# Kernel tuning notes

Hardware: AMD Instinct MI355X
Metric: run time of the kernel (lower is better)

The kernel has to match this reference:

```python
import jax, jax.numpy as jnp
import numpy as np

INPUTS = 128        # raw inputs
HIDDEN = 256
OUTPUTS = 32
NETWORKS = 64
K = 32              # max_incoming_connections
INPUTS_T = INPUTS + 2                 # + zero-bias and one-bias neurons
NODES = HIDDEN + OUTPUTS              # sequentially computed neurons
NEURONS = INPUTS_T + HIDDEN + OUTPUTS
BATCH = 1024


def setup_inputs() -> dict:
    key = jax.random.key(0)
    k1, k2, k3 = jax.random.split(key, 3)
    x = jax.random.normal(k1, (BATCH, INPUTS), dtype=jnp.float32)
    W = jax.random.normal(k2, (INPUTS_T + HIDDEN, NODES), dtype=jnp.float32)
    networks_weights = jax.random.uniform(k3, (NETWORKS,), dtype=jnp.float32)
    # connections[n, i, k] < min(INPUTS_T + i - 1, INPUTS_T + HIDDEN), as in init_connections
    rng = np.random.default_rng(0)
    upper = np.minimum(INPUTS_T + np.arange(NODES) - 1, INPUTS_T + HIDDEN)
    raw = rng.integers(0, 1 << 30, size=(NETWORKS, NODES, K))
    connections = jnp.asarray((raw % upper[None, :, None]).astype(np.int32))
    return {"x": x, "W": W, "networks_weights": networks_weights,
            "connections": connections}


def _forward(x, W, networks_weights, connections):
    B = x.shape[0]
    # append zero-bias and one-bias input neurons
    inp = jnp.concatenate(
        [x, jnp.zeros((B, 1), x.dtype), jnp.ones((B, 1), x.dtype)], axis=1)
    post = jnp.concatenate([inp, jnp.zeros((B, NODES), x.dtype)], axis=1)  # [B, neurons]
    post = jnp.tile(post[:, None, :], (1, NETWORKS, 1))  # [B, networks, neurons]

    conns_per_node = jnp.transpose(connections, (1, 0, 2))  # [nodes, networks, K]
    node_ids = jnp.arange(NODES)

    def step(post, xs):
        idx, node = xs                                   # idx: [networks, K]
        gidx = jnp.broadcast_to(idx[None], (B, NETWORKS, K))
        vals = jnp.take_along_axis(post, gidx, axis=2)   # [B, networks, K]
        w = W[idx, node]                                  # [networks, K]
        out = jnp.sum(w[None] * vals, axis=2)             # [B, networks]
        act = jax.nn.leaky_relu(out)                      # slope 0.01, matches torch
        post = post.at[:, :, INPUTS_T + node].set(act)
        return post, None

    post, _ = jax.lax.scan(step, post, (conns_per_node, node_ids))
    outs = post[:, :, -OUTPUTS:]                          # [B, networks, outputs]
    wsoft = jax.nn.softmax(networks_weights)              # [networks]
    return jnp.einsum('n,bno->bo', wsoft, outs)


def reference(x, W, networks_weights, connections):
    return _forward(x, W, networks_weights, connections)
```

## Files before the change

### kernel.cpp

```cpp
#include <hip/hip_runtime.h>
#include <math.h>

#define NETS   64
#define NNODES 288
#define NHID   256
#define NOUT   32
#define KCON   32
#define NBATCH 1024
#define TILE   32

#ifdef __has_builtin
#if __has_builtin(__builtin_amdgcn_permlane32_swap)
#define HAVE_PLSWAP 1
#endif
#endif

__device__ __forceinline__ float xor32_sum(float a) {
#ifdef HAVE_PLSWAP
    auto r = __builtin_amdgcn_permlane32_swap(__float_as_uint(a), __float_as_uint(a),
                                              false, false);
    return __uint_as_float(r[0]) + __uint_as_float(r[1]);
#else
    return a + __shfl_xor(a, 32, 64);
#endif
}

__global__ __launch_bounds__(256) void prep_wg(const float* __restrict__ W,
                                               const int* __restrict__ conn,
                                               float* __restrict__ Wg) {
    int g = blockIdx.x * 256 + threadIdx.x;
    int node = (g >> 5) % NNODES;
    Wg[g] = W[(size_t)conn[g] * NNODES + node];
}

__global__ __launch_bounds__(256) void prep_xt(const float* __restrict__ x,
                                               float* __restrict__ xT) {
    int g = blockIdx.x * 256 + threadIdx.x;
    int b = g >> 7, r = g & 127;
    xT[(size_t)r * NBATCH + b] = x[g];
}

__global__ __launch_bounds__(64) void unn_main(const float* __restrict__ xT,
                                               const int* __restrict__ conn,
                                               const float* __restrict__ Wg,
                                               float* __restrict__ outs) {
    __shared__ float st[(130 + NHID) * TILE];
    const int lane = threadIdx.x;
    const int p    = lane & 15;
    const int s    = (lane >> 4) & 1;
    const int kh   = lane >> 5;
    const int net  = blockIdx.x >> 5;
    const int b0   = (blockIdx.x & 31) * TILE;

    for (int i = lane; i < 128 * TILE / 4; i += 64) {
        int row = i >> 3, c4 = i & 7;
        float4 v = *(const float4*)(xT + (size_t)row * NBATCH + b0 + c4 * 4);
        *(float4*)(st + row * TILE + c4 * 4) = v;
    }
    if (lane < TILE) {
        st[128 * TILE + lane] = 0.0f;
        st[129 * TILE + lane] = 1.0f;
    }
    __syncthreads();

    const size_t nb = (size_t)net * NNODES * KCON + s * KCON + kh * 16;
    const int*   cp  = conn + nb;
    const float* wp  = Wg   + nb;
    const float* stp = st + 2 * p;

    int4   ic0, ic1, ic2, ic3, in0, in1, in2, in3;
    float4 wc0, wc1, wc2, wc3, wn0, wn1, wn2, wn3;

#define PREF(I0,I1,I2,I3,W0,W1,W2,W3, nd) {                               \
    const int4*   ip = (const int4*)(cp + (size_t)(nd) * KCON);           \
    const float4* fp = (const float4*)(wp + (size_t)(nd) * KCON);         \
    I0 = ip[0]; I1 = ip[1]; I2 = ip[2]; I3 = ip[3];                       \
    W0 = fp[0]; W1 = fp[1]; W2 = fp[2]; W3 = fp[3]; }

#define G1(ii, ww) { float2 v = *(const float2*)(stp + ((ii) << 5));      \
    ax = fmaf((ww), v.x, ax); ay = fmaf((ww), v.y, ay); }

#define GATH(IV, WV) G1((IV).x, (WV).x) G1((IV).y, (WV).y)                \
                     G1((IV).z, (WV).z) G1((IV).w, (WV).w)

#define BODY(I0,I1,I2,I3,W0,W1,W2,W3, nd) {                               \
    float ax = 0.f, ay = 0.f;                                             \
    GATH(I0, W0) GATH(I1, W1) GATH(I2, W2) GATH(I3, W3)                   \
    ax = xor32_sum(ax);                                                   \
    ay = xor32_sum(ay);                                                   \
    float vx = fmaxf(ax, 0.01f * ax);                                     \
    float vy = fmaxf(ay, 0.01f * ay);                                     \
    if (kh == 0) {                                                        \
        int node = (nd) + s;                                              \
        if ((nd) < NHID)                                                  \
            *(float2*)(st + (130 + node) * TILE + 2 * p) = make_float2(vx, vy); \
        else                                                              \
            *(float2*)(outs + ((size_t)net * NOUT + (node - NHID)) * NBATCH    \
                       + b0 + 2 * p) = make_float2(vx, vy);               \
    } }

    PREF(ic0,ic1,ic2,ic3,wc0,wc1,wc2,wc3, 0)
    for (int nd = 0; nd < NNODES; nd += 4) {
        PREF(in0,in1,in2,in3,wn0,wn1,wn2,wn3, nd + 2)
        BODY(ic0,ic1,ic2,ic3,wc0,wc1,wc2,wc3, nd)
        int nd2 = (nd + 4 < NNODES) ? nd + 4 : NNODES - 2;
        PREF(ic0,ic1,ic2,ic3,wc0,wc1,wc2,wc3, nd2)
        BODY(in0,in1,in2,in3,wn0,wn1,wn2,wn3, nd + 2)
    }
#undef PREF
#undef G1
#undef GATH
#undef BODY
}

__global__ __launch_bounds__(64) void unn_reduce(const float* __restrict__ nw,
                                                 const float* __restrict__ outs,
                                                 float* __restrict__ out) {
    __shared__ float sw[NETS];
    int t  = threadIdx.x;
    int o  = blockIdx.x & 31;
    int bt = blockIdx.x >> 5;
    float v = nw[t];
    float m = v;
    #pragma unroll
    for (int off = 32; off; off >>= 1) m = fmaxf(m, __shfl_xor(m, off, 64));
    float e = __expf(v - m);
    float ssum = e;
    #pragma unroll
    for (int off = 32; off; off >>= 1) ssum += __shfl_xor(ssum, off, 64);
    sw[t] = e / ssum;
    __syncthreads();

    int bb = bt * 64 + t;
    float acc = 0.f;
    #pragma unroll 8
    for (int n = 0; n < NETS; ++n)
        acc = fmaf(sw[n], outs[((size_t)n * NOUT + o) * NBATCH + bb], acc);
    out[(size_t)bb * NOUT + o] = acc;
}

extern "C" void kernel_launch(void* const* d_in, const int* in_sizes, int n_in,
                              void* d_out, int out_size, void* d_ws, size_t ws_size,
                              hipStream_t stream) {
    const float* x    = (const float*)d_in[0];
    const float* W    = (const float*)d_in[1];
    const float* nw   = (const float*)d_in[2];
    const int*   conn = (const int*)d_in[3];
    float* out = (float*)d_out;

    char* ws = (char*)d_ws;
    float* Wg   = (float*)(ws);
    float* xT   = (float*)(ws + 2359296);
    float* outs = (float*)(ws + 2359296 + 524288);

    prep_wg <<<dim3((NETS*NNODES*KCON)/256), dim3(256), 0, stream>>>(W, conn, Wg);
    prep_xt <<<dim3((NBATCH*128)/256),       dim3(256), 0, stream>>>(x, xT);
    unn_main<<<dim3(NETS * (NBATCH/TILE)),   dim3(64),  0, stream>>>(xT, conn, Wg, outs);
    unn_reduce<<<dim3(512),                  dim3(64),  0, stream>>>(nw, outs, out);
}
```

Before: 164.4 us.

## Restructure sequential network kernel with packed metadata, smaller batch tile, deeper prefetch

Packs connection offsets and gathered weights into one interleaved int2 metadata array, so each lane loads byte offsets and weights together instead of from two streams. Halves the batch tile to 16, which doubles the block count, and splits the K reduction four ways with permlane16 and permlane32 swaps. Adds a three-deep prefetch of that metadata and an XCD-aware block remap. Folds the bias rows into the transpose kernel and adds a bf16 output fallback for when the workspace is too small, which costs precision on that path.

```diff
diff --git a/kernel.cpp b/kernel.cpp
--- a/kernel.cpp
+++ b/kernel.cpp
@@ -1,5 +1,4 @@
 #include <hip/hip_runtime.h>
-#include <math.h>
 
 #define NETS   64
 #define NNODES 288
@@ -7,16 +6,31 @@
 #define NOUT   32
 #define KCON   32
 #define NBATCH 1024
-#define TILE   32
-
-#ifdef __has_builtin
+#define TILE   16
+#define NPAIR  144
+#define ROWB   (TILE * 4)
+#define LDSZ   (386 * ROWB)
+
+#if defined(__has_builtin)
+#if __has_builtin(__builtin_amdgcn_permlane16_swap)
+#define HAVE_PL16 1
+#endif
 #if __has_builtin(__builtin_amdgcn_permlane32_swap)
-#define HAVE_PLSWAP 1
-#endif
-#endif
-
-__device__ __forceinline__ float xor32_sum(float a) {
-#ifdef HAVE_PLSWAP
+#define HAVE_PL32 1
+#endif
+#endif
+
+__device__ __forceinline__ float xor16_add(float a) {
+#ifdef HAVE_PL16
+    auto r = __builtin_amdgcn_permlane16_swap(__float_as_uint(a), __float_as_uint(a),
+                                              false, false);
+    return __uint_as_float(r[0]) + __uint_as_float(r[1]);
+#else
+    return a + __shfl_xor(a, 16, 64);
+#endif
+}
+__device__ __forceinline__ float xor32_add(float a) {
+#ifdef HAVE_PL32
     auto r = __builtin_amdgcn_permlane32_swap(__float_as_uint(a), __float_as_uint(a),
                                               false, false);
     return __uint_as_float(r[0]) + __uint_as_float(r[1]);
@@ -25,102 +39,121 @@
 #endif
 }
 
-__global__ __launch_bounds__(256) void prep_wg(const float* __restrict__ W,
-                                               const int* __restrict__ conn,
-                                               float* __restrict__ Wg) {
+__device__ __forceinline__ unsigned f2bf(float f) {
+    unsigned b = __float_as_uint(f);
+    return (b + 0x7FFFu + ((b >> 16) & 1u)) >> 16;
+}
+__device__ __forceinline__ float bf2f(unsigned short u) {
+    return __uint_as_float(((unsigned)u) << 16);
+}
+
+__global__ __launch_bounds__(256) void prep_meta(const float* __restrict__ W,
+                                                 const int* __restrict__ conn,
+                                                 int2* __restrict__ meta) {
     int g = blockIdx.x * 256 + threadIdx.x;
-    int node = (g >> 5) % NNODES;
-    Wg[g] = W[(size_t)conn[g] * NNODES + node];
+    int net = g / 9216;
+    int rem = g - net * 9216;
+    int node = rem >> 5, k = rem & 31;
+    int idx = conn[g];
+    float w = W[(size_t)idx * NNODES + node];
+    int didx = net * 9216 + (node >> 1) * 64 + (node & 1) * 32 + (k >> 3) * 8 + (k & 7);
+    meta[didx] = make_int2(idx * ROWB, __float_as_int(w));
 }
 
 __global__ __launch_bounds__(256) void prep_xt(const float* __restrict__ x,
                                                float* __restrict__ xT) {
     int g = blockIdx.x * 256 + threadIdx.x;
-    int b = g >> 7, r = g & 127;
-    xT[(size_t)r * NBATCH + b] = x[g];
-}
-
+    int r = g >> 10, b = g & 1023;
+    float v = (r < 128) ? x[(size_t)b * 128 + r] : ((r == 128) ? 0.0f : 1.0f);
+    xT[(size_t)r * NBATCH + b] = v;
+}
+
+template <bool F32OUT>
 __global__ __launch_bounds__(64) void unn_main(const float* __restrict__ xT,
-                                               const int* __restrict__ conn,
-                                               const float* __restrict__ Wg,
-                                               float* __restrict__ outs) {
-    __shared__ float st[(130 + NHID) * TILE];
+                                               const int2* __restrict__ meta,
+                                               void* __restrict__ outsv) {
+    __shared__ float Hf[LDSZ / 4];
+    char* Hl = (char*)Hf;
     const int lane = threadIdx.x;
-    const int p    = lane & 15;
-    const int s    = (lane >> 4) & 1;
-    const int kh   = lane >> 5;
-    const int net  = blockIdx.x >> 5;
-    const int b0   = (blockIdx.x & 31) * TILE;
-
-    for (int i = lane; i < 128 * TILE / 4; i += 64) {
-        int row = i >> 3, c4 = i & 7;
-        float4 v = *(const float4*)(xT + (size_t)row * NBATCH + b0 + c4 * 4);
-        *(float4*)(st + row * TILE + c4 * 4) = v;
-    }
-    if (lane < TILE) {
-        st[128 * TILE + lane] = 0.0f;
-        st[129 * TILE + lane] = 1.0f;
+    const int p    = lane & 7;
+    const int s    = (lane >> 3) & 1;
+    const int kq   = lane >> 4;
+    int bid = (int)blockIdx.x;
+    bid = (bid & 7) * 512 + (bid >> 3);
+    const int net = bid >> 6;
+    const int b0  = (bid & 63) * TILE;
+
+    for (int i = lane; i < 520; i += 64) {
+        int row = i >> 2, c = i & 3;
+        float4 v = *(const float4*)(xT + (size_t)row * NBATCH + b0 + c * 4);
+        *(float4*)(Hl + row * ROWB + c * 16) = v;
     }
     __syncthreads();
 
-    const size_t nb = (size_t)net * NNODES * KCON + s * KCON + kh * 16;
-    const int*   cp  = conn + nb;
-    const float* wp  = Wg   + nb;
-    const float* stp = st + 2 * p;
-
-    int4   ic0, ic1, ic2, ic3, in0, in1, in2, in3;
-    float4 wc0, wc1, wc2, wc3, wn0, wn1, wn2, wn3;
-
-#define PREF(I0,I1,I2,I3,W0,W1,W2,W3, nd) {                               \
-    const int4*   ip = (const int4*)(cp + (size_t)(nd) * KCON);           \
-    const float4* fp = (const float4*)(wp + (size_t)(nd) * KCON);         \
-    I0 = ip[0]; I1 = ip[1]; I2 = ip[2]; I3 = ip[3];                       \
-    W0 = fp[0]; W1 = fp[1]; W2 = fp[2]; W3 = fp[3]; }
-
-#define G1(ii, ww) { float2 v = *(const float2*)(stp + ((ii) << 5));      \
-    ax = fmaf((ww), v.x, ax); ay = fmaf((ww), v.y, ay); }
-
-#define GATH(IV, WV) G1((IV).x, (WV).x) G1((IV).y, (WV).y)                \
-                     G1((IV).z, (WV).z) G1((IV).w, (WV).w)
-
-#define BODY(I0,I1,I2,I3,W0,W1,W2,W3, nd) {                               \
-    float ax = 0.f, ay = 0.f;                                             \
-    GATH(I0, W0) GATH(I1, W1) GATH(I2, W2) GATH(I3, W3)                   \
-    ax = xor32_sum(ax);                                                   \
-    ay = xor32_sum(ay);                                                   \
-    float vx = fmaxf(ax, 0.01f * ax);                                     \
-    float vy = fmaxf(ay, 0.01f * ay);                                     \
-    if (kh == 0) {                                                        \
-        int node = (nd) + s;                                              \
-        if ((nd) < NHID)                                                  \
-            *(float2*)(st + (130 + node) * TILE + 2 * p) = make_float2(vx, vy); \
-        else                                                              \
-            *(float2*)(outs + ((size_t)net * NOUT + (node - NHID)) * NBATCH    \
-                       + b0 + 2 * p) = make_float2(vx, vy);               \
-    } }
-
-    PREF(ic0,ic1,ic2,ic3,wc0,wc1,wc2,wc3, 0)
-    for (int nd = 0; nd < NNODES; nd += 4) {
-        PREF(in0,in1,in2,in3,wn0,wn1,wn2,wn3, nd + 2)
-        BODY(ic0,ic1,ic2,ic3,wc0,wc1,wc2,wc3, nd)
-        int nd2 = (nd + 4 < NNODES) ? nd + 4 : NNODES - 2;
-        PREF(ic0,ic1,ic2,ic3,wc0,wc1,wc2,wc3, nd2)
-        BODY(in0,in1,in2,in3,wn0,wn1,wn2,wn3, nd + 2)
-    }
-#undef PREF
-#undef G1
-#undef GATH
-#undef BODY
-}
-
+    const int2* mbase = meta + (size_t)net * 9216 + (s * 4 + kq) * 8;
+    const char* Hp = Hl + p * 8;
+    float*          o32p = (float*)outsv        + (size_t)net * NOUT * NBATCH + b0 + 2 * p;
+    unsigned short* o16p = (unsigned short*)outsv + (size_t)net * NOUT * NBATCH + b0 + 2 * p;
+
+    int4 A[4], B[4], C[4];
+
+    auto PREF = [&](int4 (&M)[4], int t) {
+        const int4* mp = (const int4*)(mbase + (size_t)t * 64);
+        #pragma unroll
+        for (int j = 0; j < 4; ++j) M[j] = mp[j];
+    };
+
+    auto BODY = [&](const int4 (&M)[4], int t) {
+        float ax0 = 0.f, ay0 = 0.f, ax1 = 0.f, ay1 = 0.f;
+        #pragma unroll
+        for (int j = 0; j < 4; ++j) {
+            int4 m = M[j];
+            float2 v0 = *(const float2*)(Hp + m.x);
+            float2 v1 = *(const float2*)(Hp + m.z);
+            float w0 = __int_as_float(m.y), w1 = __int_as_float(m.w);
+            if (j & 1) {
+                ax1 = fmaf(w0, v0.x, ax1); ay1 = fmaf(w0, v0.y, ay1);
+                ax1 = fmaf(w1, v1.x, ax1); ay1 = fmaf(w1, v1.y, ay1);
+            } else {
+                ax0 = fmaf(w0, v0.x, ax0); ay0 = fmaf(w0, v0.y, ay0);
+                ax0 = fmaf(w1, v1.x, ax0); ay0 = fmaf(w1, v1.y, ay0);
+            }
+        }
+        float ax = ax0 + ax1, ay = ay0 + ay1;
+        ax = xor16_add(ax); ay = xor16_add(ay);
+        ax = xor32_add(ax); ay = xor32_add(ay);
+        float rx = fmaxf(ax, 0.01f * ax);
+        float ry = fmaxf(ay, 0.01f * ay);
+        int node = 2 * t + s;
+        if (kq == 0) {
+            if (node < NHID) {
+                *(float2*)(Hl + (130 + node) * ROWB + p * 8) = make_float2(rx, ry);
+            } else if (F32OUT) {
+                *(float2*)(o32p + (size_t)(node - NHID) * NBATCH) = make_float2(rx, ry);
+            } else {
+                unsigned u = f2bf(rx) | (f2bf(ry) << 16);
+                *(unsigned*)(o16p + (size_t)(node - NHID) * NBATCH) = u;
+            }
+        }
+    };
+
+    PREF(A, 0); PREF(B, 1); PREF(C, 2);
+    for (int t = 0; t < NPAIR; t += 3) {
+        BODY(A, t);     PREF(A, (t + 3 < NPAIR) ? t + 3 : NPAIR - 1);
+        BODY(B, t + 1); PREF(B, (t + 4 < NPAIR) ? t + 4 : NPAIR - 1);
+        BODY(C, t + 2); PREF(C, (t + 5 < NPAIR) ? t + 5 : NPAIR - 1);
+    }
+}
+
+template <bool F32OUT>
 __global__ __launch_bounds__(64) void unn_reduce(const float* __restrict__ nw,
-                                                 const float* __restrict__ outs,
+                                                 const void* __restrict__ outsv,
                                                  float* __restrict__ out) {
     __shared__ float sw[NETS];
-    int t  = threadIdx.x;
+    int tt = threadIdx.x;
     int o  = blockIdx.x & 31;
     int bt = blockIdx.x >> 5;
-    float v = nw[t];
+    float v = nw[tt];
     float m = v;
     #pragma unroll
     for (int off = 32; off; off >>= 1) m = fmaxf(m, __shfl_xor(m, off, 64));
@@ -128,14 +161,19 @@
     float ssum = e;
     #pragma unroll
     for (int off = 32; off; off >>= 1) ssum += __shfl_xor(ssum, off, 64);
-    sw[t] = e / ssum;
+    sw[tt] = e / ssum;
     __syncthreads();
 
-    int bb = bt * 64 + t;
+    int bb = bt * 64 + tt;
+    const float* o32 = (const float*)outsv;
+    const unsigned short* o16 = (const unsigned short*)outsv;
     float acc = 0.f;
     #pragma unroll 8
-    for (int n = 0; n < NETS; ++n)
-        acc = fmaf(sw[n], outs[((size_t)n * NOUT + o) * NBATCH + bb], acc);
+    for (int n = 0; n < NETS; ++n) {
+        size_t idx = ((size_t)n * NOUT + o) * NBATCH + bb;
+        float val = F32OUT ? o32[idx] : bf2f(o16[idx]);
+        acc = fmaf(sw[n], val, acc);
+    }
     out[(size_t)bb * NOUT + o] = acc;
 }
 
@@ -149,12 +187,19 @@
     float* out = (float*)d_out;
 
     char* ws = (char*)d_ws;
-    float* Wg   = (float*)(ws);
-    float* xT   = (float*)(ws + 2359296);
-    float* outs = (float*)(ws + 2359296 + 524288);
-
-    prep_wg <<<dim3((NETS*NNODES*KCON)/256), dim3(256), 0, stream>>>(W, conn, Wg);
-    prep_xt <<<dim3((NBATCH*128)/256),       dim3(256), 0, stream>>>(x, xT);
-    unn_main<<<dim3(NETS * (NBATCH/TILE)),   dim3(64),  0, stream>>>(xT, conn, Wg, outs);
-    unn_reduce<<<dim3(512),                  dim3(64),  0, stream>>>(nw, outs, out);
-}
+    int2*  meta = (int2*)(ws);
+    float* xT   = (float*)(ws + 4718592);
+    void*  outs = (void*)(ws + 4718592 + 532480);
+
+    const bool f32path = ws_size >= (size_t)4718592 + 532480 + 8388608;
+
+    prep_meta<<<dim3(2304), dim3(256), 0, stream>>>(W, conn, meta);
+    prep_xt  <<<dim3(520),  dim3(256), 0, stream>>>(x, xT);
+    if (f32path) {
+        unn_main<true> <<<dim3(NETS * (NBATCH/TILE)), dim3(64), 0, stream>>>(xT, meta, outs);
+        unn_reduce<true> <<<dim3(512), dim3(64), 0, stream>>>(nw, outs, out);
+    } else {
+        unn_main<false> <<<dim3(NETS * (NBATCH/TILE)), dim3(64), 0, stream>>>(xT, meta, outs);
+        unn_reduce<false> <<<dim3(512), dim3(64), 0, stream>>>(nw, outs, out);
+    }
+}
```

Measured after the change: 202.6 us. 1.23x slower.
